# Kernel tuning notes

Measured on AMD Instinct MI355X. Metric: run time of the kernel, lower is better.

## Reference

```python
import jax, jax.numpy as jnp
import numpy as np
from jax.scipy.ndimage import map_coordinates


def _so3_exp(w):
    # Rodrigues formula, small-angle safe. w: [B,3] -> [B,3,3]
    th = jnp.linalg.norm(w, axis=-1)
    small = th < 1e-6
    ths = jnp.where(small, 1.0, th)
    A = jnp.where(small, 1.0 - th * th / 6.0, jnp.sin(ths) / ths)
    Bc = jnp.where(small, 0.5 - th * th / 24.0, (1.0 - jnp.cos(ths)) / (ths * ths))
    wx, wy, wz = w[..., 0], w[..., 1], w[..., 2]
    z = jnp.zeros_like(wx)
    K = jnp.stack([
        jnp.stack([z, -wz, wy], -1),
        jnp.stack([wz, z, -wx], -1),
        jnp.stack([-wy, wx, z], -1),
    ], -2)
    I = jnp.eye(3, dtype=w.dtype)
    return I + A[..., None, None] * K + Bc[..., None, None] * (K @ K)


def _pose(rot, xyz, rt_inv, isocenter):
    # pivot about isocenter expressed in camera frame (transform_point(rt_inv^-1, iso))
    iso_h = jnp.concatenate([isocenter, jnp.ones((1,), isocenter.dtype)])
    c = (jnp.linalg.inv(rt_inv[0]) @ iso_h)[:3]
    I4 = jnp.eye(4, dtype=rot.dtype)
    pivot = I4.at[:3, 3].set(c)
    pivot_inv = I4.at[:3, 3].set(-c)
    R = _so3_exp(rot)[0]
    t = R @ xyz[0]  # einsum('bij,bj->bi', R, xyz)
    T = I4.at[:3, :3].set(R).at[:3, 3].set(t)
    return pivot @ T @ pivot_inv


def _render(volume, k_inv, ext, sdd, height, width, n_samples):
    # DRR: cast one ray per detector pixel from the source, trilinearly sample
    # the CT volume at n_samples midpoints along source->target, accumulate.
    Rw = ext[:3, :3]
    src = ext[:3, 3]
    u = jnp.arange(width, dtype=volume.dtype) + 0.5
    v = jnp.arange(height, dtype=volume.dtype) + 0.5
    uu, vv = jnp.meshgrid(u, v, indexing='xy')  # [H,W]
    pix = jnp.stack([uu, vv, jnp.ones_like(uu)], -1)  # [H,W,3]
    dirs = jnp.einsum('ij,hwj->hwi', k_inv[0], pix)  # camera-frame ray dirs
    tgt = src + sdd[0] * jnp.einsum('ij,hwj->hwi', Rw, dirs)  # detector points in world
    seg = tgt - src  # [H,W,3]
    tvals = (jnp.arange(n_samples, dtype=volume.dtype) + 0.5) / n_samples
    pts = src + tvals[:, None, None, None] * seg[None]  # [n,H,W,3] (voxel coords)
    step = jnp.linalg.norm(seg, axis=-1) / n_samples  # [H,W] per-sample path length
    vals = map_coordinates(volume, [pts[..., 0], pts[..., 1], pts[..., 2]],
                           order=1, mode='constant', cval=0.0)  # [n,H,W]
    img = vals.sum(0) * step
    return img[None, None]  # [1,1,H,W]


def setup_inputs() -> dict:
    key = jax.random.key(0)
    k1, k2, k3 = jax.random.split(key, 3)
    D = 256
    volume = jax.random.uniform(k1, (D, D, D), dtype=jnp.float32)
    isocenter = jnp.array([128.0, 128.0, 128.0], jnp.float32)
    sdd = jnp.array([600.0], jnp.float32)
    f, cx, cy = 850.0, 256.0, 256.0
    K = jnp.array([[f, 0.0, cx], [0.0, f, cy], [0.0, 0.0, 1.0]], jnp.float32)
    k_inv = jnp.linalg.inv(K)[None]
    rt_inv = jnp.eye(4, dtype=jnp.float32).at[:3, 3].set(
        jnp.array([128.0, 128.0, -472.0], jnp.float32))[None]
    rot = 1e-8 * jax.random.normal(k2, (1, 3), jnp.float32)
    xyz = 1e-8 * jax.random.normal(k3, (1, 3), jnp.float32)
    return {"volume": volume, "isocenter": isocenter, "rt_inv": rt_inv,
            "k_inv": k_inv, "sdd": sdd, "rot": rot, "xyz": xyz,
            "height": 512, "width": 512, "n_samples": 128}


def reference(volume, isocenter, rt_inv, k_inv, sdd, rot, xyz, height, width, n_samples):
    pose = _pose(rot, xyz, rt_inv, isocenter)
    ext = rt_inv[0] @ pose  # rt_inv @ pose
    return _render(volume, k_inv, ext, sdd, height, width, n_samples)
```

## Files before the change

kernel.cpp:

```cpp
#include <hip/hip_runtime.h>
#include <math.h>

#define VD 256
#define PAIR_BYTES (VD * VD * VD * 4UL)


__device__ inline unsigned short f2bf(float f) {
    unsigned int u = __float_as_uint(f);
    u += 0x7FFFu + ((u >> 16) & 1u);
    return (unsigned short)(u >> 16);
}

__device__ inline void invert4x4(const float* m, float* inv) {
    inv[0]  =  m[5]*m[10]*m[15] - m[5]*m[11]*m[14] - m[9]*m[6]*m[15] + m[9]*m[7]*m[14] + m[13]*m[6]*m[11] - m[13]*m[7]*m[10];
    inv[4]  = -m[4]*m[10]*m[15] + m[4]*m[11]*m[14] + m[8]*m[6]*m[15] - m[8]*m[7]*m[14] - m[12]*m[6]*m[11] + m[12]*m[7]*m[10];
    inv[8]  =  m[4]*m[9]*m[15]  - m[4]*m[11]*m[13] - m[8]*m[5]*m[15] + m[8]*m[7]*m[13] + m[12]*m[5]*m[11] - m[12]*m[7]*m[9];
    inv[12] = -m[4]*m[9]*m[14]  + m[4]*m[10]*m[13] + m[8]*m[5]*m[14] - m[8]*m[6]*m[13] - m[12]*m[5]*m[10] + m[12]*m[6]*m[9];
    inv[1]  = -m[1]*m[10]*m[15] + m[1]*m[11]*m[14] + m[9]*m[2]*m[15] - m[9]*m[3]*m[14] - m[13]*m[2]*m[11] + m[13]*m[3]*m[10];
    inv[5]  =  m[0]*m[10]*m[15] - m[0]*m[11]*m[14] - m[8]*m[2]*m[15] + m[8]*m[3]*m[14] + m[12]*m[2]*m[11] - m[12]*m[3]*m[10];
    inv[9]  = -m[0]*m[9]*m[15]  + m[0]*m[11]*m[13] + m[8]*m[1]*m[15] - m[8]*m[3]*m[13] - m[12]*m[1]*m[11] + m[12]*m[3]*m[9];
    inv[13] =  m[0]*m[9]*m[14]  - m[0]*m[10]*m[13] - m[8]*m[1]*m[14] + m[8]*m[2]*m[13] + m[12]*m[1]*m[10] - m[12]*m[2]*m[9];
    inv[2]  =  m[1]*m[6]*m[15]  - m[1]*m[7]*m[14]  - m[5]*m[2]*m[15] + m[5]*m[3]*m[14] + m[13]*m[2]*m[7]  - m[13]*m[3]*m[6];
    inv[6]  = -m[0]*m[6]*m[15]  + m[0]*m[7]*m[14]  + m[4]*m[2]*m[15] - m[4]*m[3]*m[14] - m[12]*m[2]*m[7]  + m[12]*m[3]*m[6];
    inv[10] =  m[0]*m[5]*m[15]  - m[0]*m[7]*m[13]  - m[4]*m[1]*m[15] + m[4]*m[3]*m[13] + m[12]*m[1]*m[7]  - m[12]*m[3]*m[5];
    inv[14] = -m[0]*m[5]*m[14]  + m[0]*m[6]*m[13]  + m[4]*m[1]*m[14] - m[4]*m[2]*m[13] - m[12]*m[1]*m[6]  + m[12]*m[2]*m[5];
    inv[3]  = -m[1]*m[6]*m[11]  + m[1]*m[7]*m[10]  + m[5]*m[2]*m[11] - m[5]*m[3]*m[10] - m[9]*m[2]*m[7]   + m[9]*m[3]*m[6];
    inv[7]  =  m[0]*m[6]*m[11]  - m[0]*m[7]*m[10]  - m[4]*m[2]*m[11] + m[4]*m[3]*m[10] + m[8]*m[2]*m[7]   - m[8]*m[3]*m[6];
    inv[11] = -m[0]*m[5]*m[11]  + m[0]*m[7]*m[9]   + m[4]*m[1]*m[11] - m[4]*m[3]*m[9]  - m[8]*m[1]*m[7]   + m[8]*m[3]*m[5];
    inv[15] =  m[0]*m[5]*m[10]  - m[0]*m[6]*m[9]   - m[4]*m[1]*m[10] + m[4]*m[2]*m[9]  + m[8]*m[1]*m[6]   - m[8]*m[2]*m[5];
    float det = m[0]*inv[0] + m[1]*inv[4] + m[2]*inv[8] + m[3]*inv[12];
    float rdet = 1.0f / det;
    for (int i = 0; i < 16; i++) inv[i] *= rdet;
}

__global__ void setup_k(const float* __restrict__ iso,
                        const float* __restrict__ rt,
                        const float* __restrict__ kinv,
                        const float* __restrict__ sdd,
                        const float* __restrict__ rot,
                        const float* __restrict__ xyz,
                        const int* __restrict__ pH,
                        const int* __restrict__ pW,
                        float* __restrict__ P) {
    if (threadIdx.x != 0 || blockIdx.x != 0) return;
    float m[16];
    for (int i = 0; i < 16; i++) m[i] = rt[i];
    float minv[16];
    invert4x4(m, minv);
    float c0 = minv[0]*iso[0] + minv[1]*iso[1] + minv[2]*iso[2]  + minv[3];
    float c1 = minv[4]*iso[0] + minv[5]*iso[1] + minv[6]*iso[2]  + minv[7];
    float c2 = minv[8]*iso[0] + minv[9]*iso[1] + minv[10]*iso[2] + minv[11];
    float wx = rot[0], wy = rot[1], wz = rot[2];
    float th2 = wx*wx + wy*wy + wz*wz;
    float th = sqrtf(th2);
    float Ac, Bc;
    if (th < 1e-6f) { Ac = 1.0f - th2 / 6.0f; Bc = 0.5f - th2 / 24.0f; }
    else            { Ac = sinf(th) / th;     Bc = (1.0f - cosf(th)) / th2; }
    float R[9];
    R[0] = 1.0f + Bc * (-(wy*wy + wz*wz));
    R[1] = Ac * (-wz) + Bc * (wx*wy);
    R[2] = Ac * ( wy) + Bc * (wx*wz);
    R[3] = Ac * ( wz) + Bc * (wx*wy);
    R[4] = 1.0f + Bc * (-(wx*wx + wz*wz));
    R[5] = Ac * (-wx) + Bc * (wy*wz);
    R[6] = Ac * (-wy) + Bc * (wx*wz);
    R[7] = Ac * ( wx) + Bc * (wy*wz);
    R[8] = 1.0f + Bc * (-(wx*wx + wy*wy));
    float tx = R[0]*xyz[0] + R[1]*xyz[1] + R[2]*xyz[2];
    float ty = R[3]*xyz[0] + R[4]*xyz[1] + R[5]*xyz[2];
    float tz = R[6]*xyz[0] + R[7]*xyz[1] + R[8]*xyz[2];
    float pt0 = c0 + tx - (R[0]*c0 + R[1]*c1 + R[2]*c2);
    float pt1 = c1 + ty - (R[3]*c0 + R[4]*c1 + R[5]*c2);
    float pt2 = c2 + tz - (R[6]*c0 + R[7]*c1 + R[8]*c2);
    float E[12];
    for (int i = 0; i < 3; i++) {
        for (int j = 0; j < 3; j++)
            E[i*4+j] = rt[i*4+0]*R[0*3+j] + rt[i*4+1]*R[1*3+j] + rt[i*4+2]*R[2*3+j];
        E[i*4+3] = rt[i*4+0]*pt0 + rt[i*4+1]*pt1 + rt[i*4+2]*pt2 + rt[i*4+3];
    }
    float s = sdd[0];
    float M[9];
    for (int i = 0; i < 3; i++)
        for (int j = 0; j < 3; j++)
            M[i*3+j] = s * (E[i*4+0]*kinv[0*3+j] + E[i*4+1]*kinv[1*3+j] + E[i*4+2]*kinv[2*3+j]);
    for (int i = 0; i < 9; i++) P[i] = M[i];
    float src3[3] = {E[3], E[7], E[11]};
    P[9] = src3[0]; P[10] = src3[1]; P[11] = src3[2];

    float W = (float)pW[0], H = (float)pH[0];
    float us[2] = {0.5f, W - 0.5f};
    float vs[2] = {0.5f, H - 0.5f};
    for (int a = 0; a < 3; a++) {
        float gmin = 1e30f, gmax = -1e30f;
        for (int i = 0; i < 2; i++)
            for (int j = 0; j < 2; j++) {
                float g = M[a*3+0]*us[i] + M[a*3+1]*vs[j] + M[a*3+2];
                gmin = fminf(gmin, g); gmax = fmaxf(gmax, g);
            }
        float sa = src3[a];
        float lo = sa + fminf(0.0f, gmin);
        float hi = sa + fmaxf(0.0f, gmax);
        int loi = (int)floorf(lo) - 4;
        int hii = (int)ceilf(hi) + 5;
        loi = min(max(loi, 0), VD - 1);
        hii = min(max(hii, 0), VD - 1);
        P[12 + 2*a] = (float)loi;
        P[13 + 2*a] = (float)hii;
    }
}

__global__ __launch_bounds__(256)
void transpose_k(const float* __restrict__ in, unsigned int* __restrict__ Tp,
                 const float* __restrict__ P) {
    const int x0 = blockIdx.x * 64;
    const int z0 = blockIdx.y * 32;
    const int y  = blockIdx.z;
    const int xlo = (int)P[12], xhi = (int)P[13];
    const int ylo = (int)P[14], yhi = (int)P[15];
    const int zlo = (int)P[16], zhi = (int)P[17];
    if (x0 + 63 < xlo || x0 > xhi || y < ylo || y > yhi ||
        z0 + 31 < zlo || z0 > zhi) return;

    __shared__ unsigned short tile[32][68];
    const int t = threadIdx.x;
    {
        const int zq = t & 7;
        const int xl = t >> 3;
        #pragma unroll
        for (int i = 0; i < 2; i++) {
            int xr = xl + 32 * i;
            const float4 f = *(const float4*)(in + (((size_t)(x0 + xr)) << 16) + (y << 8) + z0 + 4*zq);
            tile[4*zq+0][xr] = f2bf(f.x);
            tile[4*zq+1][xr] = f2bf(f.y);
            tile[4*zq+2][xr] = f2bf(f.z);
            tile[4*zq+3][xr] = f2bf(f.w);
        }
        if (t < 8) {
            int xs = min(x0 + 64, VD - 1);
            const float4 f = *(const float4*)(in + (((size_t)xs) << 16) + (y << 8) + z0 + 4*t);
            tile[4*t+0][64] = f2bf(f.x);
            tile[4*t+1][64] = f2bf(f.y);
            tile[4*t+2][64] = f2bf(f.z);
            tile[4*t+3][64] = f2bf(f.w);
        }
    }
    __syncthreads();
    {
        const int xq = t & 15;
        const int zl = t >> 4;
        #pragma unroll
        for (int i = 0; i < 2; i++) {
            int zr = zl + 16 * i;
            unsigned int a0 = tile[zr][4*xq+0];
            unsigned int a1 = tile[zr][4*xq+1];
            unsigned int a2 = tile[zr][4*xq+2];
            unsigned int a3 = tile[zr][4*xq+3];
            unsigned int a4 = tile[zr][4*xq+4];
            uint4 o;
            o.x = a0 | (a1 << 16);
            o.y = a1 | (a2 << 16);
            o.z = a2 | (a3 << 16);
            o.w = a3 | (a4 << 16);
            *(uint4*)(Tp + (((size_t)(z0 + zr)) << 16) + (y << 8) + x0 + 4*xq) = o;
        }
    }
}

__global__ __launch_bounds__(256)
void render_pair(const unsigned int* __restrict__ Tp, const float* __restrict__ P,
                 const int* __restrict__ pW, const int* __restrict__ pN,
                 float* __restrict__ out, int total) {
    int tid = blockIdx.x * 256 + threadIdx.x;
    if (tid >= total) return;
    const int W = pW[0];
    const int N = pN[0];
    int w = tid % W;
    int h = tid / W;
    float u = (float)w + 0.5f;
    float v = (float)h + 0.5f;

    float m0 = P[0], m1 = P[1], m2 = P[2];
    float m3 = P[3], m4 = P[4], m5 = P[5];
    float m6 = P[6], m7 = P[7], m8 = P[8];
    float sx = P[9], sy = P[10], sz = P[11];

    float gx = m0*u + m1*v + m2;
    float gy = m3*u + m4*v + m5;
    float gz = m6*u + m7*v + m8;
    float len = sqrtf(gx*gx + gy*gy + gz*gz);
    float invN = 1.0f / (float)N;

    float t0 = 0.0f, t1 = 1.0f;
    {
        float s3[3] = {sx, sy, sz};
        float g3[3] = {gx, gy, gz};
        for (int a = 0; a < 3; a++) {
            float g = g3[a], s = s3[a];
            if (fabsf(g) > 1e-20f) {
                float ta = (-1.0f - s) / g;
                float tb = ((float)VD - s) / g;
                float lo = fminf(ta, tb), hi = fmaxf(ta, tb);
                t0 = fmaxf(t0, lo);
                t1 = fminf(t1, hi);
            } else if (s <= -1.0f || s >= (float)VD) {
                t1 = -1.0f;
            }
        }
    }
    int k0 = (int)floorf(t0 * (float)N - 0.5f) - 1;
    int k1 = (int)ceilf (t1 * (float)N - 0.5f) + 1;
    if (k0 < 0) k0 = 0;
    if (k1 > N - 1) k1 = N - 1;

    float acc = 0.0f;
    #pragma unroll 2
    for (int k = k0; k <= k1; k++) {
        float t = ((float)k + 0.5f) * invN;
        float x = fmaf(t, gx, sx);
        float y = fmaf(t, gy, sy);
        float z = fmaf(t, gz, sz);

        float fx = floorf(x); int ix = (int)fx; float ax = x - fx;
        float fy = floorf(y); int iy = (int)fy; float ay = y - fy;
        float fz = floorf(z); int iz = (int)fz; float az = z - fz;

        float wx0v = ((unsigned)ix       < (unsigned)VD) ? (1.0f - ax) : 0.0f;
        float wx1v = ((unsigned)(ix + 1) < (unsigned)VD) ? ax : 0.0f;
        int bx = min(max(ix, 0), VD - 1);
        int sxi = ix - bx;
        float w0p = (sxi == 0) ? wx0v : ((sxi == -1) ? wx1v : 0.0f);
        float w1p = (sxi == 0) ? wx1v : 0.0f;

        float wy0 = ((unsigned)iy       < (unsigned)VD) ? (1.0f - ay) : 0.0f;
        float wy1 = ((unsigned)(iy + 1) < (unsigned)VD) ? ay : 0.0f;
        float wz0 = ((unsigned)iz       < (unsigned)VD) ? (1.0f - az) : 0.0f;
        float wz1 = ((unsigned)(iz + 1) < (unsigned)VD) ? az : 0.0f;

        int iy0 = min(max(iy, 0), VD - 1), iy1 = min(max(iy + 1, 0), VD - 1);
        int iz0 = min(max(iz, 0), VD - 1), iz1 = min(max(iz + 1, 0), VD - 1);

        int i00 = (iz0 << 16) + (iy0 << 8) + bx;
        int i01 = i00 + ((iy1 - iy0) << 8);
        int i10 = i00 + ((iz1 - iz0) << 16);
        int i11 = i10 + ((iy1 - iy0) << 8);

        unsigned int p00 = Tp[i00];
        unsigned int p01 = Tp[i01];
        unsigned int p10 = Tp[i10];
        unsigned int p11 = Tp[i11];

        float f00a = __uint_as_float(p00 << 16), f00b = __uint_as_float(p00 & 0xFFFF0000u);
        float f01a = __uint_as_float(p01 << 16), f01b = __uint_as_float(p01 & 0xFFFF0000u);
        float f10a = __uint_as_float(p10 << 16), f10b = __uint_as_float(p10 & 0xFFFF0000u);
        float f11a = __uint_as_float(p11 << 16), f11b = __uint_as_float(p11 & 0xFFFF0000u);

        float cx00 = fmaf(f00a, w0p, f00b * w1p);
        float cx01 = fmaf(f01a, w0p, f01b * w1p);
        float cx10 = fmaf(f10a, w0p, f10b * w1p);
        float cx11 = fmaf(f11a, w0p, f11b * w1p);

        float cy0 = fmaf(cx00, wy0, cx01 * wy1);
        float cy1 = fmaf(cx10, wy0, cx11 * wy1);
        acc = fmaf(cy0, wz0, acc);
        acc = fmaf(cy1, wz1, acc);
    }
    out[tid] = acc * len * invN;
}

__global__ __launch_bounds__(256)
void render_direct(const float* __restrict__ vol, const float* __restrict__ P,
                   const int* __restrict__ pW, const int* __restrict__ pN,
                   float* __restrict__ out, int total) {
    int tid = blockIdx.x * 256 + threadIdx.x;
    if (tid >= total) return;
    const int W = pW[0];
    const int N = pN[0];
    int w = tid % W;
    int h = tid / W;
    float u = (float)w + 0.5f;
    float v = (float)h + 0.5f;
    float m0 = P[0], m1 = P[1], m2 = P[2];
    float m3 = P[3], m4 = P[4], m5 = P[5];
    float m6 = P[6], m7 = P[7], m8 = P[8];
    float sx = P[9], sy = P[10], sz = P[11];
    float gx = m0*u + m1*v + m2;
    float gy = m3*u + m4*v + m5;
    float gz = m6*u + m7*v + m8;
    float len = sqrtf(gx*gx + gy*gy + gz*gz);
    float invN = 1.0f / (float)N;
    float t0 = 0.0f, t1 = 1.0f;
    {
        float s3[3] = {sx, sy, sz};
        float g3[3] = {gx, gy, gz};
        for (int a = 0; a < 3; a++) {
            float g = g3[a], s = s3[a];
            if (fabsf(g) > 1e-20f) {
                float ta = (-1.0f - s) / g;
                float tb = ((float)VD - s) / g;
                float lo = fminf(ta, tb), hi = fmaxf(ta, tb);
                t0 = fmaxf(t0, lo);
                t1 = fminf(t1, hi);
            } else if (s <= -1.0f || s >= (float)VD) {
                t1 = -1.0f;
            }
        }
    }
    int k0 = (int)floorf(t0 * (float)N - 0.5f) - 1;
    int k1 = (int)ceilf (t1 * (float)N - 0.5f) + 1;
    if (k0 < 0) k0 = 0;
    if (k1 > N - 1) k1 = N - 1;
    float acc = 0.0f;
    for (int k = k0; k <= k1; k++) {
        float t = ((float)k + 0.5f) * invN;
        float x = fmaf(t, gx, sx);
        float y = fmaf(t, gy, sy);
        float z = fmaf(t, gz, sz);
        float fx = floorf(x); int ix = (int)fx; float ax = x - fx;
        float fy = floorf(y); int iy = (int)fy; float ay = y - fy;
        float fz = floorf(z); int iz = (int)fz; float az = z - fz;
        float wx0 = ((unsigned)ix       < (unsigned)VD) ? (1.0f - ax) : 0.0f;
        float wx1 = ((unsigned)(ix + 1) < (unsigned)VD) ? ax : 0.0f;
        float wy0 = ((unsigned)iy       < (unsigned)VD) ? (1.0f - ay) : 0.0f;
        float wy1 = ((unsigned)(iy + 1) < (unsigned)VD) ? ay : 0.0f;
        float wz0 = ((unsigned)iz       < (unsigned)VD) ? (1.0f - az) : 0.0f;
        float wz1 = ((unsigned)(iz + 1) < (unsigned)VD) ? az : 0.0f;
        int ix0 = min(max(ix, 0), VD - 1), ix1 = min(max(ix + 1, 0), VD - 1);
        int iy0 = min(max(iy, 0), VD - 1), iy1 = min(max(iy + 1, 0), VD - 1);
        int iz0 = min(max(iz, 0), VD - 1), iz1 = min(max(iz + 1, 0), VD - 1);
        int X0 = ix0 << 16, X1 = ix1 << 16;
        int Y0 = iy0 << 8,  Y1 = iy1 << 8;
        float v000 = vol[X0 + Y0 + iz0];
        float v001 = vol[X0 + Y0 + iz1];
        float v010 = vol[X0 + Y1 + iz0];
        float v011 = vol[X0 + Y1 + iz1];
        float v100 = vol[X1 + Y0 + iz0];
        float v101 = vol[X1 + Y0 + iz1];
        float v110 = vol[X1 + Y1 + iz0];
        float v111 = vol[X1 + Y1 + iz1];
        float c00 = fmaf(v000, wz0, v001 * wz1);
        float c01 = fmaf(v010, wz0, v011 * wz1);
        float c10 = fmaf(v100, wz0, v101 * wz1);
        float c11 = fmaf(v110, wz0, v111 * wz1);
        float c0  = fmaf(c00, wy0, c01 * wy1);
        float c1  = fmaf(c10, wy0, c11 * wy1);
        acc += fmaf(c0, wx0, c1 * wx1);
    }
    out[tid] = acc * len * invN;
}

extern "C" void kernel_launch(void* const* d_in, const int* in_sizes, int n_in,
                              void* d_out, int out_size, void* d_ws, size_t ws_size,
                              hipStream_t stream) {
    const float* vol  = (const float*)d_in[0];
    const float* iso  = (const float*)d_in[1];
    const float* rt   = (const float*)d_in[2];
    const float* kinv = (const float*)d_in[3];
    const float* sdd  = (const float*)d_in[4];
    const float* rot  = (const float*)d_in[5];
    const float* xyz  = (const float*)d_in[6];
    const int* pH = (const int*)d_in[7];
    const int* pW = (const int*)d_in[8];
    const int* pN = (const int*)d_in[9];
    float* out = (float*)d_out;
    int total = out_size;

    if (ws_size >= PAIR_BYTES + 256) {
        unsigned int* Tp = (unsigned int*)d_ws;
        float* P = (float*)((char*)d_ws + PAIR_BYTES);
        setup_k<<<1, 64, 0, stream>>>(iso, rt, kinv, sdd, rot, xyz, pH, pW, P);
        transpose_k<<<dim3(4, 8, 256), 256, 0, stream>>>(vol, Tp, P);
        render_pair<<<(total + 255) / 256, 256, 0, stream>>>(Tp, P, pW, pN, out, total);
    } else {
        float* P = (float*)d_ws;
        setup_k<<<1, 64, 0, stream>>>(iso, rt, kinv, sdd, rot, xyz, pH, pW, P);
        render_direct<<<(total + 255) / 256, 256, 0, stream>>>(vol, P, pW, pN, out, total);
    }
}
```

Before: 145.0 us.

## Fuse pose setup into kernels and split ray march into guarded/unguarded segments

Removes the single-thread setup kernel launch by recomputing the pose and bounding box redundantly in thread 0 of every transpose and render block, then sharing it through shared memory. The render loop computes an interior t-range where all trilinear taps are in bounds and runs a branch-free loop there with lerp-form interpolation, using guarded sampling only for head and tail samples. The transpose reads its tile with a vectorized 8-byte shared-memory load and widens the tile padding. The trade-off is redundant per-block setup math, including a 4x4 inverse done by one thread, plus extra control flow, in exchange for one fewer launch and fewer instructions per sample.

```diff
diff --git a/kernel.cpp b/kernel.cpp
--- a/kernel.cpp
+++ b/kernel.cpp
@@ -3,7 +3,6 @@
 
 #define VD 256
 #define PAIR_BYTES (VD * VD * VD * 4UL)
-
 
 __device__ inline unsigned short f2bf(float f) {
     unsigned int u = __float_as_uint(f);
@@ -33,16 +32,13 @@
     for (int i = 0; i < 16; i++) inv[i] *= rdet;
 }
 
-__global__ void setup_k(const float* __restrict__ iso,
-                        const float* __restrict__ rt,
-                        const float* __restrict__ kinv,
-                        const float* __restrict__ sdd,
-                        const float* __restrict__ rot,
-                        const float* __restrict__ xyz,
-                        const int* __restrict__ pH,
-                        const int* __restrict__ pW,
-                        float* __restrict__ P) {
-    if (threadIdx.x != 0 || blockIdx.x != 0) return;
+__device__ inline void compute_pose(const float* __restrict__ iso,
+                                    const float* __restrict__ rt,
+                                    const float* __restrict__ kinv,
+                                    const float* __restrict__ sdd,
+                                    const float* __restrict__ rot,
+                                    const float* __restrict__ xyz,
+                                    float* M, float* src3) {
     float m[16];
     for (int i = 0; i < 16; i++) m[i] = rt[i];
     float minv[16];
@@ -79,50 +75,48 @@
         E[i*4+3] = rt[i*4+0]*pt0 + rt[i*4+1]*pt1 + rt[i*4+2]*pt2 + rt[i*4+3];
     }
     float s = sdd[0];
-    float M[9];
     for (int i = 0; i < 3; i++)
         for (int j = 0; j < 3; j++)
             M[i*3+j] = s * (E[i*4+0]*kinv[0*3+j] + E[i*4+1]*kinv[1*3+j] + E[i*4+2]*kinv[2*3+j]);
-    for (int i = 0; i < 9; i++) P[i] = M[i];
-    float src3[3] = {E[3], E[7], E[11]};
-    P[9] = src3[0]; P[10] = src3[1]; P[11] = src3[2];
-
-    float W = (float)pW[0], H = (float)pH[0];
-    float us[2] = {0.5f, W - 0.5f};
-    float vs[2] = {0.5f, H - 0.5f};
-    for (int a = 0; a < 3; a++) {
-        float gmin = 1e30f, gmax = -1e30f;
-        for (int i = 0; i < 2; i++)
-            for (int j = 0; j < 2; j++) {
-                float g = M[a*3+0]*us[i] + M[a*3+1]*vs[j] + M[a*3+2];
-                gmin = fminf(gmin, g); gmax = fmaxf(gmax, g);
-            }
-        float sa = src3[a];
-        float lo = sa + fminf(0.0f, gmin);
-        float hi = sa + fmaxf(0.0f, gmax);
-        int loi = (int)floorf(lo) - 4;
-        int hii = (int)ceilf(hi) + 5;
-        loi = min(max(loi, 0), VD - 1);
-        hii = min(max(hii, 0), VD - 1);
-        P[12 + 2*a] = (float)loi;
-        P[13 + 2*a] = (float)hii;
-    }
+    src3[0] = E[3]; src3[1] = E[7]; src3[2] = E[11];
 }
 
 __global__ __launch_bounds__(256)
 void transpose_k(const float* __restrict__ in, unsigned int* __restrict__ Tp,
-                 const float* __restrict__ P) {
+                 const float* __restrict__ iso, const float* __restrict__ rt,
+                 const float* __restrict__ kinv, const float* __restrict__ sdd,
+                 const float* __restrict__ rot, const float* __restrict__ xyz,
+                 const int* __restrict__ pH, const int* __restrict__ pW) {
+    __shared__ int B[6];
+    __shared__ unsigned short tile[32][72];
+    const int t = threadIdx.x;
+    if (t == 0) {
+        float M[9], src3[3];
+        compute_pose(iso, rt, kinv, sdd, rot, xyz, M, src3);
+        float W = (float)pW[0], H = (float)pH[0];
+        float us[2] = {0.5f, W - 0.5f};
+        float vs[2] = {0.5f, H - 0.5f};
+        for (int a = 0; a < 3; a++) {
+            float gmin = 1e30f, gmax = -1e30f;
+            for (int i = 0; i < 2; i++)
+                for (int j = 0; j < 2; j++) {
+                    float g = M[a*3+0]*us[i] + M[a*3+1]*vs[j] + M[a*3+2];
+                    gmin = fminf(gmin, g); gmax = fmaxf(gmax, g);
+                }
+            float sa = src3[a];
+            int loi = (int)floorf(sa + fminf(0.0f, gmin)) - 4;
+            int hii = (int)ceilf (sa + fmaxf(0.0f, gmax)) + 5;
+            B[2*a]   = min(max(loi, 0), VD - 1);
+            B[2*a+1] = min(max(hii, 0), VD - 1);
+        }
+    }
+    __syncthreads();
     const int x0 = blockIdx.x * 64;
     const int z0 = blockIdx.y * 32;
     const int y  = blockIdx.z;
-    const int xlo = (int)P[12], xhi = (int)P[13];
-    const int ylo = (int)P[14], yhi = (int)P[15];
-    const int zlo = (int)P[16], zhi = (int)P[17];
-    if (x0 + 63 < xlo || x0 > xhi || y < ylo || y > yhi ||
-        z0 + 31 < zlo || z0 > zhi) return;
-
-    __shared__ unsigned short tile[32][68];
-    const int t = threadIdx.x;
+    if (x0 + 63 < B[0] || x0 > B[1] || y < B[2] || y > B[3] ||
+        z0 + 31 < B[4] || z0 > B[5]) return;
+
     {
         const int zq = t & 7;
         const int xl = t >> 3;
@@ -151,10 +145,9 @@
         #pragma unroll
         for (int i = 0; i < 2; i++) {
             int zr = zl + 16 * i;
-            unsigned int a0 = tile[zr][4*xq+0];
-            unsigned int a1 = tile[zr][4*xq+1];
-            unsigned int a2 = tile[zr][4*xq+2];
-            unsigned int a3 = tile[zr][4*xq+3];
+            const uint2 aa = *reinterpret_cast<const uint2*>(&tile[zr][4*xq]);
+            unsigned int a0 = aa.x & 0xFFFFu, a1 = aa.x >> 16;
+            unsigned int a2 = aa.y & 0xFFFFu, a3 = aa.y >> 16;
             unsigned int a4 = tile[zr][4*xq+4];
             uint4 o;
             o.x = a0 | (a1 << 16);
@@ -166,10 +159,67 @@
     }
 }
 
+__device__ inline float sample_guarded(const unsigned int* __restrict__ Tp,
+                                       float x, float y, float z) {
+    float fx = floorf(x); int ix = (int)fx; float ax = x - fx;
+    float fy = floorf(y); int iy = (int)fy; float ay = y - fy;
+    float fz = floorf(z); int iz = (int)fz; float az = z - fz;
+
+    float wx0v = ((unsigned)ix       < (unsigned)VD) ? (1.0f - ax) : 0.0f;
+    float wx1v = ((unsigned)(ix + 1) < (unsigned)VD) ? ax : 0.0f;
+    int bx = min(max(ix, 0), VD - 1);
+    int sxi = ix - bx;
+    float w0p = (sxi == 0) ? wx0v : ((sxi == -1) ? wx1v : 0.0f);
+    float w1p = (sxi == 0) ? wx1v : 0.0f;
+
+    float wy0 = ((unsigned)iy       < (unsigned)VD) ? (1.0f - ay) : 0.0f;
+    float wy1 = ((unsigned)(iy + 1) < (unsigned)VD) ? ay : 0.0f;
+    float wz0 = ((unsigned)iz       < (unsigned)VD) ? (1.0f - az) : 0.0f;
+    float wz1 = ((unsigned)(iz + 1) < (unsigned)VD) ? az : 0.0f;
+
+    int iy0 = min(max(iy, 0), VD - 1), iy1 = min(max(iy + 1, 0), VD - 1);
+    int iz0 = min(max(iz, 0), VD - 1), iz1 = min(max(iz + 1, 0), VD - 1);
+
+    int i00 = (iz0 << 16) + (iy0 << 8) + bx;
+    int i01 = i00 + ((iy1 - iy0) << 8);
+    int i10 = i00 + ((iz1 - iz0) << 16);
+    int i11 = i10 + ((iy1 - iy0) << 8);
+
+    unsigned int p00 = Tp[i00];
+    unsigned int p01 = Tp[i01];
+    unsigned int p10 = Tp[i10];
+    unsigned int p11 = Tp[i11];
+
+    float f00a = __uint_as_float(p00 << 16), f00b = __uint_as_float(p00 & 0xFFFF0000u);
+    float f01a = __uint_as_float(p01 << 16), f01b = __uint_as_float(p01 & 0xFFFF0000u);
+    float f10a = __uint_as_float(p10 << 16), f10b = __uint_as_float(p10 & 0xFFFF0000u);
+    float f11a = __uint_as_float(p11 << 16), f11b = __uint_as_float(p11 & 0xFFFF0000u);
+
+    float cx00 = fmaf(f00a, w0p, f00b * w1p);
+    float cx01 = fmaf(f01a, w0p, f01b * w1p);
+    float cx10 = fmaf(f10a, w0p, f10b * w1p);
+    float cx11 = fmaf(f11a, w0p, f11b * w1p);
+
+    float cy0 = fmaf(cx00, wy0, cx01 * wy1);
+    float cy1 = fmaf(cx10, wy0, cx11 * wy1);
+    return cy0 * wz0 + cy1 * wz1;
+}
+
 __global__ __launch_bounds__(256)
-void render_pair(const unsigned int* __restrict__ Tp, const float* __restrict__ P,
+void render_pair(const unsigned int* __restrict__ Tp,
+                 const float* __restrict__ iso, const float* __restrict__ rt,
+                 const float* __restrict__ kinv, const float* __restrict__ sdd,
+                 const float* __restrict__ rot, const float* __restrict__ xyz,
                  const int* __restrict__ pW, const int* __restrict__ pN,
                  float* __restrict__ out, int total) {
+    __shared__ float S[12];
+    if (threadIdx.x == 0) {
+        float M[9], src3[3];
+        compute_pose(iso, rt, kinv, sdd, rot, xyz, M, src3);
+        for (int i = 0; i < 9; i++) S[i] = M[i];
+        S[9] = src3[0]; S[10] = src3[1]; S[11] = src3[2];
+    }
+    __syncthreads();
     int tid = blockIdx.x * 256 + threadIdx.x;
     if (tid >= total) return;
     const int W = pW[0];
@@ -179,31 +229,34 @@
     float u = (float)w + 0.5f;
     float v = (float)h + 0.5f;
 
-    float m0 = P[0], m1 = P[1], m2 = P[2];
-    float m3 = P[3], m4 = P[4], m5 = P[5];
-    float m6 = P[6], m7 = P[7], m8 = P[8];
-    float sx = P[9], sy = P[10], sz = P[11];
-
-    float gx = m0*u + m1*v + m2;
-    float gy = m3*u + m4*v + m5;
-    float gz = m6*u + m7*v + m8;
+    float gx = S[0]*u + S[1]*v + S[2];
+    float gy = S[3]*u + S[4]*v + S[5];
+    float gz = S[6]*u + S[7]*v + S[8];
+    float sx = S[9], sy = S[10], sz = S[11];
     float len = sqrtf(gx*gx + gy*gy + gz*gz);
     float invN = 1.0f / (float)N;
 
     float t0 = 0.0f, t1 = 1.0f;
+    float tA = 0.0f, tB = 1.0f;
     {
+        const float HI = (float)(VD - 1) - 0.01f;
         float s3[3] = {sx, sy, sz};
         float g3[3] = {gx, gy, gz};
         for (int a = 0; a < 3; a++) {
             float g = g3[a], s = s3[a];
             if (fabsf(g) > 1e-20f) {
-                float ta = (-1.0f - s) / g;
-                float tb = ((float)VD - s) / g;
-                float lo = fminf(ta, tb), hi = fmaxf(ta, tb);
-                t0 = fmaxf(t0, lo);
-                t1 = fminf(t1, hi);
-            } else if (s <= -1.0f || s >= (float)VD) {
-                t1 = -1.0f;
+                float rg = 1.0f / g;
+                float ta = (-1.0f - s) * rg;
+                float tb = ((float)VD - s) * rg;
+                t0 = fmaxf(t0, fminf(ta, tb));
+                t1 = fminf(t1, fmaxf(ta, tb));
+                float tc = (0.0f - s) * rg;
+                float td = (HI - s) * rg;
+                tA = fmaxf(tA, fminf(tc, td));
+                tB = fminf(tB, fmaxf(tc, td));
+            } else {
+                if (s <= -1.0f || s >= (float)VD) t1 = -1.0f;
+                if (s < 0.0f || s > HI)           tB = -2.0f;
             }
         }
     }
@@ -211,66 +264,66 @@
     int k1 = (int)ceilf (t1 * (float)N - 0.5f) + 1;
     if (k0 < 0) k0 = 0;
     if (k1 > N - 1) k1 = N - 1;
+    int kA = (int)ceilf (tA * (float)N - 0.5f) + 1;
+    int kB = (int)floorf(tB * (float)N - 0.5f) - 1;
+    kA = max(kA, k0);
+    kB = min(kB, k1);
 
     float acc = 0.0f;
+    int headEnd = min(kA - 1, k1);
+    for (int k = k0; k <= headEnd; k++) {
+        float t = ((float)k + 0.5f) * invN;
+        acc += sample_guarded(Tp, fmaf(t, gx, sx), fmaf(t, gy, sy), fmaf(t, gz, sz));
+    }
     #pragma unroll 2
-    for (int k = k0; k <= k1; k++) {
+    for (int k = kA; k <= kB; k++) {
         float t = ((float)k + 0.5f) * invN;
         float x = fmaf(t, gx, sx);
         float y = fmaf(t, gy, sy);
         float z = fmaf(t, gz, sz);
-
         float fx = floorf(x); int ix = (int)fx; float ax = x - fx;
         float fy = floorf(y); int iy = (int)fy; float ay = y - fy;
         float fz = floorf(z); int iz = (int)fz; float az = z - fz;
-
-        float wx0v = ((unsigned)ix       < (unsigned)VD) ? (1.0f - ax) : 0.0f;
-        float wx1v = ((unsigned)(ix + 1) < (unsigned)VD) ? ax : 0.0f;
-        int bx = min(max(ix, 0), VD - 1);
-        int sxi = ix - bx;
-        float w0p = (sxi == 0) ? wx0v : ((sxi == -1) ? wx1v : 0.0f);
-        float w1p = (sxi == 0) ? wx1v : 0.0f;
-
-        float wy0 = ((unsigned)iy       < (unsigned)VD) ? (1.0f - ay) : 0.0f;
-        float wy1 = ((unsigned)(iy + 1) < (unsigned)VD) ? ay : 0.0f;
-        float wz0 = ((unsigned)iz       < (unsigned)VD) ? (1.0f - az) : 0.0f;
-        float wz1 = ((unsigned)(iz + 1) < (unsigned)VD) ? az : 0.0f;
-
-        int iy0 = min(max(iy, 0), VD - 1), iy1 = min(max(iy + 1, 0), VD - 1);
-        int iz0 = min(max(iz, 0), VD - 1), iz1 = min(max(iz + 1, 0), VD - 1);
-
-        int i00 = (iz0 << 16) + (iy0 << 8) + bx;
-        int i01 = i00 + ((iy1 - iy0) << 8);
-        int i10 = i00 + ((iz1 - iz0) << 16);
-        int i11 = i10 + ((iy1 - iy0) << 8);
-
-        unsigned int p00 = Tp[i00];
-        unsigned int p01 = Tp[i01];
-        unsigned int p10 = Tp[i10];
-        unsigned int p11 = Tp[i11];
-
+        int idx = (iz << 16) + (iy << 8) + ix;
+        unsigned int p00 = Tp[idx];
+        unsigned int p01 = Tp[idx + 256];
+        unsigned int p10 = Tp[idx + 65536];
+        unsigned int p11 = Tp[idx + 65536 + 256];
         float f00a = __uint_as_float(p00 << 16), f00b = __uint_as_float(p00 & 0xFFFF0000u);
         float f01a = __uint_as_float(p01 << 16), f01b = __uint_as_float(p01 & 0xFFFF0000u);
         float f10a = __uint_as_float(p10 << 16), f10b = __uint_as_float(p10 & 0xFFFF0000u);
         float f11a = __uint_as_float(p11 << 16), f11b = __uint_as_float(p11 & 0xFFFF0000u);
-
-        float cx00 = fmaf(f00a, w0p, f00b * w1p);
-        float cx01 = fmaf(f01a, w0p, f01b * w1p);
-        float cx10 = fmaf(f10a, w0p, f10b * w1p);
-        float cx11 = fmaf(f11a, w0p, f11b * w1p);
-
-        float cy0 = fmaf(cx00, wy0, cx01 * wy1);
-        float cy1 = fmaf(cx10, wy0, cx11 * wy1);
-        acc = fmaf(cy0, wz0, acc);
-        acc = fmaf(cy1, wz1, acc);
+        float cx00 = fmaf(f00b - f00a, ax, f00a);
+        float cx01 = fmaf(f01b - f01a, ax, f01a);
+        float cx10 = fmaf(f10b - f10a, ax, f10a);
+        float cx11 = fmaf(f11b - f11a, ax, f11a);
+        float cy0 = fmaf(cx01 - cx00, ay, cx00);
+        float cy1 = fmaf(cx11 - cx10, ay, cx10);
+        acc += fmaf(cy1 - cy0, az, cy0);
+    }
+    int tailStart = max(kB + 1, kA);
+    for (int k = tailStart; k <= k1; k++) {
+        float t = ((float)k + 0.5f) * invN;
+        acc += sample_guarded(Tp, fmaf(t, gx, sx), fmaf(t, gy, sy), fmaf(t, gz, sz));
     }
     out[tid] = acc * len * invN;
 }
 
 __global__ __launch_bounds__(256)
-void render_direct(const float* __restrict__ vol, const float* __restrict__ P,
+void render_direct(const float* __restrict__ vol,
+                   const float* __restrict__ iso, const float* __restrict__ rt,
+                   const float* __restrict__ kinv, const float* __restrict__ sdd,
+                   const float* __restrict__ rot, const float* __restrict__ xyz,
                    const int* __restrict__ pW, const int* __restrict__ pN,
                    float* __restrict__ out, int total) {
+    __shared__ float S[12];
+    if (threadIdx.x == 0) {
+        float M[9], src3[3];
+        compute_pose(iso, rt, kinv, sdd, rot, xyz, M, src3);
+        for (int i = 0; i < 9; i++) S[i] = M[i];
+        S[9] = src3[0]; S[10] = src3[1]; S[11] = src3[2];
+    }
+    __syncthreads();
     int tid = blockIdx.x * 256 + threadIdx.x;
     if (tid >= total) return;
     const int W = pW[0];
@@ -279,38 +332,14 @@
     int h = tid / W;
     float u = (float)w + 0.5f;
     float v = (float)h + 0.5f;
-    float m0 = P[0], m1 = P[1], m2 = P[2];
-    float m3 = P[3], m4 = P[4], m5 = P[5];
-    float m6 = P[6], m7 = P[7], m8 = P[8];
-    float sx = P[9], sy = P[10], sz = P[11];
-    float gx = m0*u + m1*v + m2;
-    float gy = m3*u + m4*v + m5;
-    float gz = m6*u + m7*v + m8;
+    float gx = S[0]*u + S[1]*v + S[2];
+    float gy = S[3]*u + S[4]*v + S[5];
+    float gz = S[6]*u + S[7]*v + S[8];
+    float sx = S[9], sy = S[10], sz = S[11];
     float len = sqrtf(gx*gx + gy*gy + gz*gz);
     float invN = 1.0f / (float)N;
-    float t0 = 0.0f, t1 = 1.0f;
-    {
-        float s3[3] = {sx, sy, sz};
-        float g3[3] = {gx, gy, gz};
-        for (int a = 0; a < 3; a++) {
-            float g = g3[a], s = s3[a];
-            if (fabsf(g) > 1e-20f) {
-                float ta = (-1.0f - s) / g;
-                float tb = ((float)VD - s) / g;
-                float lo = fminf(ta, tb), hi = fmaxf(ta, tb);
-                t0 = fmaxf(t0, lo);
-                t1 = fminf(t1, hi);
-            } else if (s <= -1.0f || s >= (float)VD) {
-                t1 = -1.0f;
-            }
-        }
-    }
-    int k0 = (int)floorf(t0 * (float)N - 0.5f) - 1;
-    int k1 = (int)ceilf (t1 * (float)N - 0.5f) + 1;
-    if (k0 < 0) k0 = 0;
-    if (k1 > N - 1) k1 = N - 1;
     float acc = 0.0f;
-    for (int k = k0; k <= k1; k++) {
+    for (int k = 0; k < N; k++) {
         float t = ((float)k + 0.5f) * invN;
         float x = fmaf(t, gx, sx);
         float y = fmaf(t, gy, sy);
@@ -364,15 +393,11 @@
     float* out = (float*)d_out;
     int total = out_size;
 
-    if (ws_size >= PAIR_BYTES + 256) {
+    if (ws_size >= PAIR_BYTES) {
         unsigned int* Tp = (unsigned int*)d_ws;
-        float* P = (float*)((char*)d_ws + PAIR_BYTES);
-        setup_k<<<1, 64, 0, stream>>>(iso, rt, kinv, sdd, rot, xyz, pH, pW, P);
-        transpose_k<<<dim3(4, 8, 256), 256, 0, stream>>>(vol, Tp, P);
-        render_pair<<<(total + 255) / 256, 256, 0, stream>>>(Tp, P, pW, pN, out, total);
+        transpose_k<<<dim3(4, 8, 256), 256, 0, stream>>>(vol, Tp, iso, rt, kinv, sdd, rot, xyz, pH, pW);
+        render_pair<<<(total + 255) / 256, 256, 0, stream>>>(Tp, iso, rt, kinv, sdd, rot, xyz, pW, pN, out, total);
     } else {
-        float* P = (float*)d_ws;
-        setup_k<<<1, 64, 0, stream>>>(iso, rt, kinv, sdd, rot, xyz, pH, pW, P);
-        render_direct<<<(total + 255) / 256, 256, 0, stream>>>(vol, P, pW, pN, out, total);
-    }
-}
+        render_direct<<<(total + 255) / 256, 256, 0, stream>>>(vol, iso, rt, kinv, sdd, rot, xyz, pW, pN, out, total);
+    }
+}
```

New measurement: 143.4 us, median of 2. Within noise of the previous version (-1.2%).
